# Performance work log

Measured on AMD Instinct MI355X. Metric: run time of the kernel, lower is better.

The kernel has to match this reference:

```python
import jax, jax.numpy as jnp
from jax import lax
import numpy as np

Bn, DM, HH, WW = 2, 192, 64, 64   # batch, d_model, H, W (H==W required by transpose-stack)
DI = 384   # d_inner = ssm_ratio * d_model
DS = 16    # ssm_d_state
ND = 4     # n_directions
CG = 12    # c_group
LN_EPS = 1e-5


def setup_inputs() -> dict:
    key = jax.random.key(0)
    k = jax.random.split(key, 16)
    w = lambda i, shape: jax.random.normal(k[i], shape, jnp.float32) * 0.05
    return {
        "x": jax.random.normal(k[0], (Bn, DM, HH, WW), jnp.float32),
        "in_proj_w": w(1, (DI, DM)),
        "dwconv_w": w(2, (DI, 1, 3, 3)),
        "dwconv_b": w(3, (DI,)),
        "x_down_w": w(4, (DS, DI)),
        "w_up_w": w(5, (CG * DI, DS)),
        "l_up_w": w(6, (ND * DI, DS)),
        "u_up_w": w(7, (ND * DI, DS)),
        "d_up_w": w(8, (ND * DI, DS)),
        "m_w": w(9, (ND,)),
        "grn_gamma": w(10, (DI,)),
        "grn_beta": w(11, (DI,)),
        "norm_w": 1.0 + w(12, (DI,)),
        "norm_b": w(13, (DI,)),
        "out_proj_w": w(14, (DM, DI)),
    }


def _conv1x1(w, x):
    return jnp.einsum('oc,bchw->bohw', w, x)


def _gate_recurrent(X, B, G1, G2, G3):
    # H[:, :, h, w] = B*X + G1*H[h-1,w-1] + G2*H[h,w-1] + G3*H[h+1,w-1]
    # sequential over width; vectorized over batch/channel/height via a column scan.
    def step(hprev, col):  # hprev: [B, C, H]
        xw, bw, g1w, g2w, g3w = col
        z = jnp.zeros_like(hprev[:, :, :1])
        up = jnp.concatenate([z, hprev[:, :, :-1]], axis=2)   # H[h-1, w-1]
        dn = jnp.concatenate([hprev[:, :, 1:], z], axis=2)    # H[h+1, w-1]
        h = bw * xw + g1w * up + g2w * hprev + g3w * dn
        return h, h

    cols = tuple(jnp.moveaxis(t, 3, 0) for t in (X, B, G1, G2, G3))  # [W, B, C, H]
    h0 = jnp.zeros(X.shape[:3], X.dtype)
    _, ys = lax.scan(step, h0, cols)
    return jnp.moveaxis(ys, 0, 3)  # [B, C, H, W]


def _normalize_w(Gl, Gm, Gr):
    gl, gm, gr = jax.nn.sigmoid(Gl), jax.nn.sigmoid(Gm), jax.nn.sigmoid(Gr)
    s = gl + gm + gr
    s = s.at[:, :, 0, :].set(gm[:, :, 0, :] + gr[:, :, 0, :])
    s = s.at[:, :, -1, :].set(gl[:, :, -1, :] + gm[:, :, -1, :])
    s = jnp.maximum(s, 1e-7)
    return gl / s, gm / s, gr / s


def reference(x, in_proj_w, dwconv_w, dwconv_b, x_down_w, w_up_w, l_up_w, u_up_w,
              d_up_w, m_w, grn_gamma, grn_beta, norm_w, norm_b, out_proj_w):
    Bsz = x.shape[0]
    # in_proj (1x1, no bias) + SiLU + depthwise 3x3 conv
    h = jax.nn.silu(_conv1x1(in_proj_w, x))
    h = lax.conv_general_dilated(h, dwconv_w, (1, 1), ((1, 1), (1, 1)),
                                 feature_group_count=DI) + dwconv_b[None, :, None, None]
    # forward_corev1
    xp = _conv1x1(x_down_w, h)            # [B, DS, H, W]
    ws = _conv1x1(w_up_w, xp)             # [B, 12*DI, H, W]
    Ls = _conv1x1(l_up_w, xp)             # [B, 4*DI, H, W]
    Us = _conv1x1(u_up_w, xp)
    Ds = _conv1x1(d_up_w, xp)
    hT = jnp.swapaxes(h, 2, 3)            # requires H==W
    xs = jnp.concatenate([h, hT, h[..., ::-1], hT[..., ::-1]], axis=1)  # [B, 4*DI, H, W]
    G1, G2, G3 = jnp.split(ws, 3, axis=1)
    g1, g2, g3 = _normalize_w(G1, G2, G3)
    out = _gate_recurrent(xs, Ls, g1, g2, g3)
    out = out * Us + xs * Ds
    # merge directions: view [B, 4, DI*H, W], 1x1 conv 4->1
    out = out.reshape(Bsz, ND, DI * HH, WW)
    y = jnp.einsum('d,bdxw->bxw', m_w, out).reshape(Bsz, DI, HH, WW)
    # LayerNorm2d over channel dim
    mu = y.mean(axis=1, keepdims=True)
    var = ((y - mu) ** 2).mean(axis=1, keepdims=True)
    y = (y - mu) * lax.rsqrt(var + LN_EPS) * norm_w[None, :, None, None] + norm_b[None, :, None, None]
    # GRN
    Gx = jnp.sqrt(jnp.sum(y * y, axis=(2, 3), keepdims=True))        # [B, C, 1, 1]
    Nx = Gx / (Gx.mean(axis=1, keepdims=True) + 1e-6)
    y = grn_gamma[None, :, None, None] * (y * Nx) + grn_beta[None, :, None, None] + y
    # out_proj (1x1, no bias)
    return _conv1x1(out_proj_w, y)
```

## Files before the change

### kernel.cpp

```cpp
#include <hip/hip_runtime.h>
#include <math.h>

#define Bn 2
#define DM 192
#define DI 384
#define DS 16
#define HH 64
#define WW 64
#define HW 4096
#define ND 4

__device__ __forceinline__ float fastrcp(float x) { return __builtin_amdgcn_rcpf(x); }
__device__ __forceinline__ float fsig(float x) {
    return fastrcp(1.0f + __expf(-x));
}

#define WLANE(r, s, L) asm("v_writelane_b32 %0, %1, " #L : "+v"(r) : "s"(s))

__device__ __forceinline__ float shift_up(float x) {
    int xi = __float_as_int(x);
    int r = __builtin_amdgcn_mov_dpp(xi, 0x111, 0xF, 0xF, true);
    int t15 = __builtin_amdgcn_readlane(xi, 15);
    int t31 = __builtin_amdgcn_readlane(xi, 31);
    int t47 = __builtin_amdgcn_readlane(xi, 47);
    WLANE(r, t15, 16);
    WLANE(r, t31, 32);
    WLANE(r, t47, 48);
    return __int_as_float(r);
}
__device__ __forceinline__ float shift_dn(float x) {
    int xi = __float_as_int(x);
    int r = __builtin_amdgcn_mov_dpp(xi, 0x101, 0xF, 0xF, true);
    int t16 = __builtin_amdgcn_readlane(xi, 16);
    int t32 = __builtin_amdgcn_readlane(xi, 32);
    int t48 = __builtin_amdgcn_readlane(xi, 48);
    WLANE(r, t16, 15);
    WLANE(r, t32, 31);
    WLANE(r, t48, 47);
    return __int_as_float(r);
}

__global__ __launch_bounds__(256, 3) void k_inproj(const float* __restrict__ x,
                                                   const float* __restrict__ w,
                                                   float* __restrict__ hpre) {
    int og = blockIdx.y, b = blockIdx.z;
    int p = blockIdx.x * 256 + threadIdx.x;
    const float* wr = w + (size_t)og * 16 * DM;
    const float* xb = x + (size_t)b * DM * HW + p;
    float acc[16];
#pragma unroll
    for (int j = 0; j < 16; ++j) acc[j] = 0.f;
    for (int c = 0; c < DM; c += 4) {
        float x0 = xb[(size_t)(c + 0) * HW];
        float x1 = xb[(size_t)(c + 1) * HW];
        float x2 = xb[(size_t)(c + 2) * HW];
        float x3 = xb[(size_t)(c + 3) * HW];
#pragma unroll
        for (int j = 0; j < 16; ++j) {
            const float* wj = wr + j * DM + c;
            acc[j] = fmaf(wj[0], x0, fmaf(wj[1], x1, fmaf(wj[2], x2, fmaf(wj[3], x3, acc[j]))));
        }
    }
    float* hb = hpre + (size_t)b * DI * HW + (size_t)(og * 16) * HW + p;
#pragma unroll
    for (int j = 0; j < 16; ++j) {
        float v = acc[j];
        hb[(size_t)j * HW] = v * fastrcp(1.0f + __expf(-v));
    }
}

__global__ __launch_bounds__(256) void k_dwconv(const float* __restrict__ hpre,
                                                const float* __restrict__ w,
                                                const float* __restrict__ bias,
                                                float* __restrict__ h) {
    int c = blockIdx.y, b = blockIdx.z;
    int p = blockIdx.x * 256 + threadIdx.x;
    int i = p >> 6, j = p & 63;
    const float* wp = w + c * 9;
    const float* src = hpre + ((size_t)b * DI + c) * HW;
    float acc = bias[c];
#pragma unroll
    for (int di = -1; di <= 1; ++di) {
        int ii = i + di;
        if (ii < 0 || ii >= HH) continue;
#pragma unroll
        for (int dj = -1; dj <= 1; ++dj) {
            int jj = j + dj;
            if (jj < 0 || jj >= WW) continue;
            acc = fmaf(wp[(di + 1) * 3 + (dj + 1)], src[ii * WW + jj], acc);
        }
    }
    h[((size_t)b * DI + c) * HW + p] = acc;
}

__global__ __launch_bounds__(256) void k_xdown(const float* __restrict__ h,
                                               const float* __restrict__ w,
                                               float* __restrict__ xpt) {
    __shared__ float red[4][64][17];
    int tid = threadIdx.x;
    int px = tid & 63, cw = tid >> 6;
    int gp = blockIdx.x * 64 + px;
    int b = gp >> 12, p = gp & 4095;
    const float* hb = h + (size_t)b * DI * HW + p;
    int c0 = cw * 96;
    float a[16];
#pragma unroll
    for (int s = 0; s < 16; ++s) a[s] = 0.f;
    for (int cc = 0; cc < 96; cc += 4) {
        float h0 = hb[(size_t)(c0 + cc + 0) * HW];
        float h1 = hb[(size_t)(c0 + cc + 1) * HW];
        float h2 = hb[(size_t)(c0 + cc + 2) * HW];
        float h3 = hb[(size_t)(c0 + cc + 3) * HW];
#pragma unroll
        for (int s = 0; s < 16; ++s) {
            const float* ws = w + (size_t)s * DI + c0 + cc;
            a[s] = fmaf(ws[0], h0, fmaf(ws[1], h1, fmaf(ws[2], h2, fmaf(ws[3], h3, a[s]))));
        }
    }
#pragma unroll
    for (int s = 0; s < 16; ++s) red[cw][px][s] = a[s];
    __syncthreads();
    int sg = tid >> 6;
    float4 r;
    float* o = &r.x;
#pragma unroll
    for (int j = 0; j < 4; ++j) {
        int s = sg * 4 + j;
        o[j] = red[0][px][s] + red[1][px][s] + red[2][px][s] + red[3][px][s];
    }
    int hp = p >> 6, wp_ = p & 63;
    reinterpret_cast<float4*>(xpt)[(size_t)b * (HW * 4) + (wp_ * 4 + sg) * 64 + hp] = r;
}

#define DOT16(W, q0, q1, q2, q3) \
    fmaf(W[15], q3.w, fmaf(W[14], q3.z, fmaf(W[13], q3.y, fmaf(W[12], q3.x, \
    fmaf(W[11], q2.w, fmaf(W[10], q2.z, fmaf(W[9],  q2.y, fmaf(W[8],  q2.x, \
    fmaf(W[7],  q1.w, fmaf(W[6],  q1.z, fmaf(W[5],  q1.y, fmaf(W[4],  q1.x, \
    fmaf(W[3],  q0.w, fmaf(W[2],  q0.z, fmaf(W[1],  q0.y, W[0] * q0.x)))))))))))))))

__global__ __launch_bounds__(256, 3) void k_scan(const float* __restrict__ h,
                                                 const float* __restrict__ xpt,
                                                 const float* __restrict__ wup,
                                                 const float* __restrict__ lup,
                                                 const float* __restrict__ uup,
                                                 const float* __restrict__ dup,
                                                 const float* __restrict__ mw,
                                                 float* __restrict__ y) {
    int c = blockIdx.x, b = blockIdx.y;
    int tid = threadIdx.x;
    int d = tid >> 6, hl = tid & 63;

    __shared__ float htile[64][65];
    __shared__ float acc[64][65];

    const float* hb = h + ((size_t)b * DI + c) * HW;
    for (int i = tid; i < HW; i += 256) {
        htile[i >> 6][i & 63] = hb[i];
        acc[i >> 6][i & 63] = 0.f;
    }

    int row = d * DI + c;
    const float* p1 = wup + (size_t)row * DS;
    const float* p2 = wup + (size_t)(4 * DI + row) * DS;
    const float* p3 = wup + (size_t)(8 * DI + row) * DS;
    const float* pL = lup + (size_t)row * DS;
    const float* pU = uup + (size_t)row * DS;
    const float* pD = dup + (size_t)row * DS;
    float md = mw[d];
    float w1[16], w2[16], w3[16], wL[16], wU[16], wD[16];
#pragma unroll
    for (int s = 0; s < 16; ++s) {
        w1[s] = p1[s]; w2[s] = p2[s]; w3[s] = p3[s];
        wL[s] = pL[s]; wU[s] = md * pU[s]; wD[s] = md * pD[s];
    }

    int xstep = (d & 1) ? 65 : 1;
    int xbase = (d & 1) ? hl : hl * 65;
    if (d & 2) { xbase += xstep * 63; xstep = -xstep; }
    const float* xptr = &htile[0][0] + xbase;

    bool isTop = (hl == 0), isBot = (hl == 63);
    float topMul = isTop ? 0.f : 1.f;
    float botMul = isBot ? 0.f : 1.f;

    float* accp = &acc[hl][0];

    const float4* xg = reinterpret_cast<const float4*>(xpt) + (size_t)b * (HW * 4) + hl;

#define LOADQ(R0, R1, R2, R3, wcol) { \
    const float4* pp_ = xg + (size_t)(wcol) * 256; \
    R0 = pp_[0]; R1 = pp_[64]; R2 = pp_[128]; R3 = pp_[192]; }

#define PREP(g1S, g2S, g3S, invS, LS, US, DvS, XS, R0, R1, R2, R3) { \
    g1S = DOT16(w1, R0, R1, R2, R3); \
    g2S = DOT16(w2, R0, R1, R2, R3); \
    g3S = DOT16(w3, R0, R1, R2, R3); \
    LS  = DOT16(wL, R0, R1, R2, R3); \
    US  = DOT16(wU, R0, R1, R2, R3); \
    DvS = DOT16(wD, R0, R1, R2, R3); \
    g1S = fsig(g1S); g2S = fsig(g2S); g3S = fsig(g3S); \
    float ss_ = fmaf(g1S, topMul, fmaf(g3S, botMul, g2S)); \
    invS = fastrcp(fmaxf(ss_, 1e-7f)); \
    XS = *xptr; xptr += xstep; }

#define COMB(g1S, g2S, g3S, invS, LS, US, DvS, XS) { \
    float upv_ = topMul * shift_up(hprev); \
    float dnv_ = botMul * shift_dn(hprev); \
    float hnew_ = fmaf(LS, XS, invS * fmaf(g1S, upv_, fmaf(g2S, hprev, g3S * dnv_))); \
    atomicAdd(accp, fmaf(hnew_, US, XS * DvS)); accp += 1; \
    hprev = hnew_; }

    float4 A0, A1, A2, A3, B0, B1, B2, B3;
    float g1a, g2a, g3a, inva, La, Ua, Dva, Xa;
    float g1b, g2b, g3b, invb, Lb, Ub, Dvb, Xb;
    float hprev = 0.f;

    LOADQ(A0, A1, A2, A3, 0);
    __syncthreads();
    LOADQ(B0, B1, B2, B3, 1);

    for (int w = 0; w < 64; w += 2) {
        PREP(g1a, g2a, g3a, inva, La, Ua, Dva, Xa, A0, A1, A2, A3);
        int wn2 = (w + 2 < 64) ? w + 2 : 63;
        LOADQ(A0, A1, A2, A3, wn2);
        COMB(g1a, g2a, g3a, inva, La, Ua, Dva, Xa);
        PREP(g1b, g2b, g3b, invb, Lb, Ub, Dvb, Xb, B0, B1, B2, B3);
        int wn3 = (w + 3 < 64) ? w + 3 : 63;
        LOADQ(B0, B1, B2, B3, wn3);
        COMB(g1b, g2b, g3b, invb, Lb, Ub, Dvb, Xb);
    }
#undef LOADQ
#undef PREP
#undef COMB

    __syncthreads();
    float* yb = y + ((size_t)b * DI + c) * HW;
    for (int i = tid; i < HW; i += 256) yb[i] = acc[i >> 6][i & 63];
}

__global__ __launch_bounds__(256) void k_ln(float* __restrict__ y,
                                            const float* __restrict__ nw,
                                            const float* __restrict__ nb) {
    int lpx = threadIdx.x & 15, chunk = threadIdx.x >> 4;
    int gp = blockIdx.x * 16 + lpx;
    int b = gp >> 12, p = gp & 4095;
    float* yb = y + (size_t)b * DI * HW + p;

    float vv[24];
    float s = 0.f, s2 = 0.f;
#pragma unroll
    for (int ci = 0; ci < 24; ++ci) {
        float v = yb[(size_t)(chunk * 24 + ci) * HW];
        vv[ci] = v;
        s += v;
        s2 = fmaf(v, v, s2);
    }
    __shared__ float S[16][17], S2[16][17];
    S[chunk][lpx] = s;
    S2[chunk][lpx] = s2;
    __syncthreads();
    float ts = 0.f, ts2 = 0.f;
#pragma unroll
    for (int k = 0; k < 16; ++k) { ts += S[k][lpx]; ts2 += S2[k][lpx]; }
    float mu = ts * (1.0f / DI);
    float var = ts2 * (1.0f / DI) - mu * mu;
    float inv = rsqrtf(var + 1e-5f);
#pragma unroll
    for (int ci = 0; ci < 24; ++ci) {
        int cch = chunk * 24 + ci;
        float v = (vv[ci] - mu) * inv;
        yb[(size_t)cch * HW] = fmaf(v, nw[cch], nb[cch]);
    }
}

__global__ __launch_bounds__(256) void k_grnsum(const float* __restrict__ y,
                                                float* __restrict__ gx) {
    int c = blockIdx.x, b = blockIdx.y;
    const float* yb = y + ((size_t)b * DI + c) * HW;
    float s = 0.f;
#pragma unroll 4
    for (int i = threadIdx.x; i < HW; i += 256) {
        float v = yb[i];
        s = fmaf(v, v, s);
    }
#pragma unroll
    for (int o = 32; o > 0; o >>= 1) s += __shfl_down(s, o);
    __shared__ float red[4];
    int wid = threadIdx.x >> 6;
    if ((threadIdx.x & 63) == 0) red[wid] = s;
    __syncthreads();
    if (threadIdx.x == 0) gx[b * DI + c] = sqrtf(red[0] + red[1] + red[2] + red[3]);
}

__global__ __launch_bounds__(256) void k_grnscale(const float* __restrict__ gxv,
                                                  const float* __restrict__ gamma,
                                                  float* __restrict__ sc) {
    int b = blockIdx.x;
    const float* g = gxv + b * DI;
    int cidx = threadIdx.x;
    float gx0 = g[cidx];
    float gx1 = (cidx < DI - 256) ? g[cidx + 256] : 0.f;
    float s = gx0 + gx1;
#pragma unroll
    for (int o = 32; o > 0; o >>= 1) s += __shfl_down(s, o);
    __shared__ float red[4];
    __shared__ float meanv;
    int wid = threadIdx.x >> 6;
    if ((threadIdx.x & 63) == 0) red[wid] = s;
    __syncthreads();
    if (threadIdx.x == 0) meanv = (red[0] + red[1] + red[2] + red[3]) * (1.0f / DI);
    __syncthreads();
    float m = meanv + 1e-6f;
    sc[b * DI + cidx] = 1.0f + gamma[cidx] * (gx0 / m);
    if (cidx < DI - 256)
        sc[b * DI + cidx + 256] = 1.0f + gamma[cidx + 256] * (gx1 / m);
}

__global__ __launch_bounds__(256, 3) void k_outproj(const float* __restrict__ y,
                                                    const float* __restrict__ w,
                                                    const float* __restrict__ sc_all,
                                                    const float* __restrict__ beta,
                                                    float* __restrict__ out) {
    int og = blockIdx.y, b = blockIdx.z;
    int p = blockIdx.x * 256 + threadIdx.x;
    const float* wr = w + (size_t)og * 8 * DI;
    const float* scb = sc_all + b * DI;
    const float* yb = y + (size_t)b * DI * HW + p;
    float acc[8];
#pragma unroll
    for (int j = 0; j < 8; ++j) acc[j] = 0.f;
    for (int c = 0; c < DI; c += 4) {
        float v0 = fmaf(yb[(size_t)(c + 0) * HW], scb[c + 0], beta[c + 0]);
        float v1 = fmaf(yb[(size_t)(c + 1) * HW], scb[c + 1], beta[c + 1]);
        float v2 = fmaf(yb[(size_t)(c + 2) * HW], scb[c + 2], beta[c + 2]);
        float v3 = fmaf(yb[(size_t)(c + 3) * HW], scb[c + 3], beta[c + 3]);
#pragma unroll
        for (int j = 0; j < 8; ++j) {
            const float* wj = wr + j * DI + c;
            acc[j] = fmaf(wj[0], v0, fmaf(wj[1], v1, fmaf(wj[2], v2, fmaf(wj[3], v3, acc[j]))));
        }
    }
    float* ob = out + (size_t)b * DM * HW + (size_t)(og * 8) * HW + p;
#pragma unroll
    for (int j = 0; j < 8; ++j) ob[(size_t)j * HW] = acc[j];
}

extern "C" void kernel_launch(void* const* d_in, const int* in_sizes, int n_in,
                              void* d_out, int out_size, void* d_ws, size_t ws_size,
                              hipStream_t stream) {
    (void)in_sizes; (void)n_in; (void)out_size; (void)ws_size;
    const float* x          = (const float*)d_in[0];
    const float* in_proj_w  = (const float*)d_in[1];
    const float* dwconv_w   = (const float*)d_in[2];
    const float* dwconv_b   = (const float*)d_in[3];
    const float* x_down_w   = (const float*)d_in[4];
    const float* w_up_w     = (const float*)d_in[5];
    const float* l_up_w     = (const float*)d_in[6];
    const float* u_up_w     = (const float*)d_in[7];
    const float* d_up_w     = (const float*)d_in[8];
    const float* m_w        = (const float*)d_in[9];
    const float* grn_gamma  = (const float*)d_in[10];
    const float* grn_beta   = (const float*)d_in[11];
    const float* norm_w     = (const float*)d_in[12];
    const float* norm_b     = (const float*)d_in[13];
    const float* out_proj_w = (const float*)d_in[14];

    float* ws = (float*)d_ws;
    const size_t NBIG = (size_t)Bn * DI * HW;
    float* hpre = ws;
    float* hbuf = ws + NBIG;
    float* xpt  = ws + 2 * NBIG;
    float* gx   = ws + 2 * NBIG + (size_t)Bn * HW * DS;
    float* sc   = gx + Bn * DI;
    float* y    = hpre;

    k_inproj<<<dim3(16, 24, 2), 256, 0, stream>>>(x, in_proj_w, hpre);
    k_dwconv<<<dim3(16, DI, Bn), 256, 0, stream>>>(hpre, dwconv_w, dwconv_b, hbuf);
    k_xdown<<<dim3(128), 256, 0, stream>>>(hbuf, x_down_w, xpt);
    k_scan<<<dim3(DI, Bn), 256, 0, stream>>>(hbuf, xpt, w_up_w, l_up_w, u_up_w,
                                             d_up_w, m_w, y);
    k_ln<<<dim3(512), 256, 0, stream>>>(y, norm_w, norm_b);
    k_grnsum<<<dim3(DI, Bn), 256, 0, stream>>>(y, gx);
    k_grnscale<<<dim3(Bn), 256, 0, stream>>>(gx, grn_gamma, sc);
    k_outproj<<<dim3(16, 24, 2), 256, 0, stream>>>(y, out_proj_w, sc, grn_beta,
                                                   (float*)d_out);
}
```

Baseline: 203.3 us.

## Pack two scan directions per thread using packed float2 FMA in k_scan

Result: slower. 235.8 us (+16.0%).

```diff
diff --git a/kernel.cpp b/kernel.cpp
--- a/kernel.cpp
+++ b/kernel.cpp
@@ -9,6 +9,9 @@
 #define WW 64
 #define HW 4096
 #define ND 4
+
+typedef __attribute__((ext_vector_type(2))) float v2f;
+union Q4 { float4 f4; v2f v2[2]; };
 
 __device__ __forceinline__ float fastrcp(float x) { return __builtin_amdgcn_rcpf(x); }
 __device__ __forceinline__ float fsig(float x) {
@@ -132,13 +135,31 @@
     reinterpret_cast<float4*>(xpt)[(size_t)b * (HW * 4) + (wp_ * 4 + sg) * 64 + hp] = r;
 }
 
-#define DOT16(W, q0, q1, q2, q3) \
-    fmaf(W[15], q3.w, fmaf(W[14], q3.z, fmaf(W[13], q3.y, fmaf(W[12], q3.x, \
-    fmaf(W[11], q2.w, fmaf(W[10], q2.z, fmaf(W[9],  q2.y, fmaf(W[8],  q2.x, \
-    fmaf(W[7],  q1.w, fmaf(W[6],  q1.z, fmaf(W[5],  q1.y, fmaf(W[4],  q1.x, \
-    fmaf(W[3],  q0.w, fmaf(W[2],  q0.z, fmaf(W[1],  q0.y, W[0] * q0.x)))))))))))))))
-
-__global__ __launch_bounds__(256, 3) void k_scan(const float* __restrict__ h,
+#define SPL(e) ((v2f){(e), (e)})
+
+__device__ __forceinline__ v2f dot16v(const v2f* __restrict__ W,
+                                      const Q4& a0, const Q4& a1,
+                                      const Q4& a2, const Q4& a3) {
+    v2f t0 = W[0] * SPL(a0.f4.x);
+    v2f t1 = W[1] * SPL(a0.f4.y);
+    t0 = __builtin_elementwise_fma(W[2],  SPL(a0.f4.z), t0);
+    t1 = __builtin_elementwise_fma(W[3],  SPL(a0.f4.w), t1);
+    t0 = __builtin_elementwise_fma(W[4],  SPL(a1.f4.x), t0);
+    t1 = __builtin_elementwise_fma(W[5],  SPL(a1.f4.y), t1);
+    t0 = __builtin_elementwise_fma(W[6],  SPL(a1.f4.z), t0);
+    t1 = __builtin_elementwise_fma(W[7],  SPL(a1.f4.w), t1);
+    t0 = __builtin_elementwise_fma(W[8],  SPL(a2.f4.x), t0);
+    t1 = __builtin_elementwise_fma(W[9],  SPL(a2.f4.y), t1);
+    t0 = __builtin_elementwise_fma(W[10], SPL(a2.f4.z), t0);
+    t1 = __builtin_elementwise_fma(W[11], SPL(a2.f4.w), t1);
+    t0 = __builtin_elementwise_fma(W[12], SPL(a3.f4.x), t0);
+    t1 = __builtin_elementwise_fma(W[13], SPL(a3.f4.y), t1);
+    t0 = __builtin_elementwise_fma(W[14], SPL(a3.f4.z), t0);
+    t1 = __builtin_elementwise_fma(W[15], SPL(a3.f4.w), t1);
+    return t0 + t1;
+}
+
+__global__ __launch_bounds__(128, 1) void k_scan(const float* __restrict__ h,
                                                  const float* __restrict__ xpt,
                                                  const float* __restrict__ wup,
                                                  const float* __restrict__ lup,
@@ -148,36 +169,46 @@
                                                  float* __restrict__ y) {
     int c = blockIdx.x, b = blockIdx.y;
     int tid = threadIdx.x;
-    int d = tid >> 6, hl = tid & 63;
+    int pr = tid >> 6, hl = tid & 63;
 
     __shared__ float htile[64][65];
     __shared__ float acc[64][65];
 
     const float* hb = h + ((size_t)b * DI + c) * HW;
-    for (int i = tid; i < HW; i += 256) {
+    for (int i = tid; i < HW; i += 128) {
         htile[i >> 6][i & 63] = hb[i];
         acc[i >> 6][i & 63] = 0.f;
     }
 
-    int row = d * DI + c;
-    const float* p1 = wup + (size_t)row * DS;
-    const float* p2 = wup + (size_t)(4 * DI + row) * DS;
-    const float* p3 = wup + (size_t)(8 * DI + row) * DS;
-    const float* pL = lup + (size_t)row * DS;
-    const float* pU = uup + (size_t)row * DS;
-    const float* pD = dup + (size_t)row * DS;
-    float md = mw[d];
-    float w1[16], w2[16], w3[16], wL[16], wU[16], wD[16];
+    int rowA = pr * DI + c, rowB = (pr + 2) * DI + c;
+    const float* a1 = wup + (size_t)rowA * DS;
+    const float* b1 = wup + (size_t)rowB * DS;
+    const float* a2 = wup + (size_t)(4 * DI + rowA) * DS;
+    const float* b2 = wup + (size_t)(4 * DI + rowB) * DS;
+    const float* a3 = wup + (size_t)(8 * DI + rowA) * DS;
+    const float* b3 = wup + (size_t)(8 * DI + rowB) * DS;
+    const float* aL = lup + (size_t)rowA * DS;
+    const float* bL = lup + (size_t)rowB * DS;
+    const float* aU = uup + (size_t)rowA * DS;
+    const float* bU = uup + (size_t)rowB * DS;
+    const float* aD = dup + (size_t)rowA * DS;
+    const float* bD = dup + (size_t)rowB * DS;
+    float mdA = mw[pr], mdB = mw[pr + 2];
+    v2f w1p[16], w2p[16], w3p[16], wLp[16], wUp[16], wDp[16];
 #pragma unroll
     for (int s = 0; s < 16; ++s) {
-        w1[s] = p1[s]; w2[s] = p2[s]; w3[s] = p3[s];
-        wL[s] = pL[s]; wU[s] = md * pU[s]; wD[s] = md * pD[s];
-    }
-
-    int xstep = (d & 1) ? 65 : 1;
-    int xbase = (d & 1) ? hl : hl * 65;
-    if (d & 2) { xbase += xstep * 63; xstep = -xstep; }
-    const float* xptr = &htile[0][0] + xbase;
+        w1p[s] = (v2f){a1[s], b1[s]};
+        w2p[s] = (v2f){a2[s], b2[s]};
+        w3p[s] = (v2f){a3[s], b3[s]};
+        wLp[s] = (v2f){aL[s], bL[s]};
+        wUp[s] = (v2f){mdA * aU[s], mdB * bU[s]};
+        wDp[s] = (v2f){mdA * aD[s], mdB * bD[s]};
+    }
+
+    int xstep = pr ? 65 : 1;
+    int xbase = pr ? hl : hl * 65;
+    const float* xptrA = &htile[0][0] + xbase;
+    const float* xptrB = &htile[0][0] + xbase + xstep * 63;
 
     bool isTop = (hl == 0), isBot = (hl == 63);
     float topMul = isTop ? 0.f : 1.f;
@@ -189,45 +220,55 @@
 
 #define LOADQ(R0, R1, R2, R3, wcol) { \
     const float4* pp_ = xg + (size_t)(wcol) * 256; \
-    R0 = pp_[0]; R1 = pp_[64]; R2 = pp_[128]; R3 = pp_[192]; }
-
-#define PREP(g1S, g2S, g3S, invS, LS, US, DvS, XS, R0, R1, R2, R3) { \
-    g1S = DOT16(w1, R0, R1, R2, R3); \
-    g2S = DOT16(w2, R0, R1, R2, R3); \
-    g3S = DOT16(w3, R0, R1, R2, R3); \
-    LS  = DOT16(wL, R0, R1, R2, R3); \
-    US  = DOT16(wU, R0, R1, R2, R3); \
-    DvS = DOT16(wD, R0, R1, R2, R3); \
-    g1S = fsig(g1S); g2S = fsig(g2S); g3S = fsig(g3S); \
-    float ss_ = fmaf(g1S, topMul, fmaf(g3S, botMul, g2S)); \
-    invS = fastrcp(fmaxf(ss_, 1e-7f)); \
-    XS = *xptr; xptr += xstep; }
-
-#define COMB(g1S, g2S, g3S, invS, LS, US, DvS, XS) { \
-    float upv_ = topMul * shift_up(hprev); \
-    float dnv_ = botMul * shift_dn(hprev); \
-    float hnew_ = fmaf(LS, XS, invS * fmaf(g1S, upv_, fmaf(g2S, hprev, g3S * dnv_))); \
-    atomicAdd(accp, fmaf(hnew_, US, XS * DvS)); accp += 1; \
-    hprev = hnew_; }
-
-    float4 A0, A1, A2, A3, B0, B1, B2, B3;
-    float g1a, g2a, g3a, inva, La, Ua, Dva, Xa;
-    float g1b, g2b, g3b, invb, Lb, Ub, Dvb, Xb;
-    float hprev = 0.f;
+    R0.f4 = pp_[0]; R1.f4 = pp_[64]; R2.f4 = pp_[128]; R3.f4 = pp_[192]; }
+
+#define PREP(g1S, g2S, g3S, LS, US, DvS, iAS, iBS, XAS, XBS, R0, R1, R2, R3) { \
+    g1S = dot16v(w1p, R0, R1, R2, R3); \
+    g2S = dot16v(w2p, R0, R1, R2, R3); \
+    g3S = dot16v(w3p, R0, R1, R2, R3); \
+    LS  = dot16v(wLp, R0, R1, R2, R3); \
+    US  = dot16v(wUp, R0, R1, R2, R3); \
+    DvS = dot16v(wDp, R0, R1, R2, R3); \
+    g1S = (v2f){fsig(g1S.x), fsig(g1S.y)}; \
+    g2S = (v2f){fsig(g2S.x), fsig(g2S.y)}; \
+    g3S = (v2f){fsig(g3S.x), fsig(g3S.y)}; \
+    float ssA_ = fmaf(g1S.x, topMul, fmaf(g3S.x, botMul, g2S.x)); \
+    float ssB_ = fmaf(g1S.y, topMul, fmaf(g3S.y, botMul, g2S.y)); \
+    iAS = fastrcp(fmaxf(ssA_, 1e-7f)); \
+    iBS = fastrcp(fmaxf(ssB_, 1e-7f)); \
+    XAS = *xptrA; xptrA += xstep; \
+    XBS = *xptrB; xptrB -= xstep; }
+
+#define COMB(g1S, g2S, g3S, LS, US, DvS, iAS, iBS, XAS, XBS) { \
+    float upA_ = topMul * shift_up(hprevA); \
+    float dnA_ = botMul * shift_dn(hprevA); \
+    float upB_ = topMul * shift_up(hprevB); \
+    float dnB_ = botMul * shift_dn(hprevB); \
+    float hnA_ = fmaf(LS.x, XAS, iAS * fmaf(g1S.x, upA_, fmaf(g2S.x, hprevA, g3S.x * dnA_))); \
+    float hnB_ = fmaf(LS.y, XBS, iBS * fmaf(g1S.y, upB_, fmaf(g2S.y, hprevB, g3S.y * dnB_))); \
+    atomicAdd(accp, fmaf(hnA_, US.x, XAS * DvS.x) + fmaf(hnB_, US.y, XBS * DvS.y)); \
+    accp += 1; \
+    hprevA = hnA_; hprevB = hnB_; }
+
+    Q4 A0, A1, A2, A3, B0, B1, B2, B3;
+    v2f g1a, g2a, g3a, La, Ua, Dva;
+    v2f g1b, g2b, g3b, Lb, Ub, Dvb;
+    float iAa, iBa, XAa, XBa, iAb, iBb, XAb, XBb;
+    float hprevA = 0.f, hprevB = 0.f;
 
     LOADQ(A0, A1, A2, A3, 0);
     __syncthreads();
     LOADQ(B0, B1, B2, B3, 1);
 
     for (int w = 0; w < 64; w += 2) {
-        PREP(g1a, g2a, g3a, inva, La, Ua, Dva, Xa, A0, A1, A2, A3);
+        PREP(g1a, g2a, g3a, La, Ua, Dva, iAa, iBa, XAa, XBa, A0, A1, A2, A3);
         int wn2 = (w + 2 < 64) ? w + 2 : 63;
         LOADQ(A0, A1, A2, A3, wn2);
-        COMB(g1a, g2a, g3a, inva, La, Ua, Dva, Xa);
-        PREP(g1b, g2b, g3b, invb, Lb, Ub, Dvb, Xb, B0, B1, B2, B3);
+        COMB(g1a, g2a, g3a, La, Ua, Dva, iAa, iBa, XAa, XBa);
+        PREP(g1b, g2b, g3b, Lb, Ub, Dvb, iAb, iBb, XAb, XBb, B0, B1, B2, B3);
         int wn3 = (w + 3 < 64) ? w + 3 : 63;
         LOADQ(B0, B1, B2, B3, wn3);
-        COMB(g1b, g2b, g3b, invb, Lb, Ub, Dvb, Xb);
+        COMB(g1b, g2b, g3b, Lb, Ub, Dvb, iAb, iBb, XAb, XBb);
     }
 #undef LOADQ
 #undef PREP
@@ -235,7 +276,7 @@
 
     __syncthreads();
     float* yb = y + ((size_t)b * DI + c) * HW;
-    for (int i = tid; i < HW; i += 256) yb[i] = acc[i >> 6][i & 63];
+    for (int i = tid; i < HW; i += 128) yb[i] = acc[i >> 6][i & 63];
 }
 
 __global__ __launch_bounds__(256) void k_ln(float* __restrict__ y,
@@ -377,7 +418,7 @@
     k_inproj<<<dim3(16, 24, 2), 256, 0, stream>>>(x, in_proj_w, hpre);
     k_dwconv<<<dim3(16, DI, Bn), 256, 0, stream>>>(hpre, dwconv_w, dwconv_b, hbuf);
     k_xdown<<<dim3(128), 256, 0, stream>>>(hbuf, x_down_w, xpt);
-    k_scan<<<dim3(DI, Bn), 256, 0, stream>>>(hbuf, xpt, w_up_w, l_up_w, u_up_w,
+    k_scan<<<dim3(DI, Bn), 128, 0, stream>>>(hbuf, xpt, w_up_w, l_up_w, u_up_w,
                                              d_up_w, m_w, y);
     k_ln<<<dim3(512), 256, 0, stream>>>(y, norm_w, norm_b);
     k_grnsum<<<dim3(DI, Bn), 256, 0, stream>>>(y, gx);
```
